# Performance work log

Hardware: AMD Instinct MI355X
Metric: run time of the kernel (lower is better)

Reference implementation:

```python
import jax, jax.numpy as jnp
import numpy as np

B, LQ, LK = 4, 2048, 2048
XS, YS, PD = 1024, 1024, 128


def setup_inputs() -> dict:
    key = jax.random.key(0)
    ks = jax.random.split(key, 8)
    s_x = 1.0 / np.sqrt(XS)
    s_y = 1.0 / np.sqrt(YS)
    return {
        "x": jax.random.normal(ks[0], (B, LQ, XS), dtype=jnp.float32),
        "y": jax.random.normal(ks[1], (B, LK, YS), dtype=jnp.float32),
        "Wq": jax.random.normal(ks[2], (XS, PD), dtype=jnp.float32) * s_x,
        "bq": jax.random.normal(ks[3], (PD,), dtype=jnp.float32) * 0.01,
        "Wk": jax.random.normal(ks[4], (YS, PD), dtype=jnp.float32) * s_y,
        "bk": jax.random.normal(ks[5], (PD,), dtype=jnp.float32) * 0.01,
        "Wv": jax.random.normal(ks[6], (YS, PD), dtype=jnp.float32) * s_y,
        "bv": jax.random.normal(ks[7], (PD,), dtype=jnp.float32) * 0.01,
        "mask": 1,
    }


def reference(x, y, Wq, bq, Wk, bk, Wv, bv, mask):
    # Projections (torch Linear: x @ W^T + b; here weights stored as [in, out])
    q = x @ Wq + bq  # [B, LQ, PD]
    k = y @ Wk + bk  # [B, LK, PD]
    v = y @ Wv + bv  # [B, LK, PD]
    scale = 1.0 / jnp.sqrt(jnp.asarray(PD, dtype=q.dtype))
    att = jax.nn.softmax(jnp.einsum("bqd,bkd->bqk", q, k) * scale, axis=-1)
    if mask:
        # NOTE: faithful to original — triu applied AFTER softmax (diagonal=1),
        # zeroing the lower triangle + diagonal without renormalizing.
        att = jnp.triu(att, k=1)
    return jnp.einsum("bqk,bkd->bqd", att, v)  # [B, LQ, PD]
```

## Files before the change

kernel.cpp:

```cpp
#include <hip/hip_runtime.h>

typedef short s8v __attribute__((ext_vector_type(8)));
typedef float f4v __attribute__((ext_vector_type(4)));

#define NB 4
#define LQ 2048
#define LKK 2048
#define XS 1024
#define PDD 128

#define PST 68
#define AST 132

__device__ __forceinline__ ushort f2bf(float x) {
  union { float f; uint u; } v; v.f = x;
  uint r = (v.u + 0x7fffu + ((v.u >> 16) & 1u)) >> 16;
  return (ushort)r;
}


__global__ __launch_bounds__(256) void k_wtrans(const float* __restrict__ Wq,
                                                const float* __restrict__ Wk,
                                                const float* __restrict__ Wv,
                                                ushort* __restrict__ Wt) {
  int p = blockIdx.y;
  const float* W = (p == 0) ? Wq : (p == 1) ? Wk : Wv;
  ushort* out = Wt + (size_t)p * (PDD * XS);
  int t = threadIdx.x;
  int n = t >> 1;
  int kk0 = (t & 1) * 16;
  int k0 = blockIdx.x * 32;
  ushort tmp[16];
#pragma unroll
  for (int i = 0; i < 16; ++i) tmp[i] = f2bf(W[(size_t)(k0 + kk0 + i) * PDD + n]);
  uint4 u0, u1;
  u0.x = tmp[0] | ((uint)tmp[1] << 16);  u0.y = tmp[2] | ((uint)tmp[3] << 16);
  u0.z = tmp[4] | ((uint)tmp[5] << 16);  u0.w = tmp[6] | ((uint)tmp[7] << 16);
  u1.x = tmp[8] | ((uint)tmp[9] << 16);  u1.y = tmp[10] | ((uint)tmp[11] << 16);
  u1.z = tmp[12] | ((uint)tmp[13] << 16); u1.w = tmp[14] | ((uint)tmp[15] << 16);
  int ct = n >> 4, lc = n & 15, kq = k0 >> 5;
  ushort* base = out + ((size_t)(ct * 32 + kq)) * 512 + (kk0 >> 3) * 128 + lc * 8;
  *(uint4*)base = u0;
  *(uint4*)(base + 128) = u1;
}

__global__ __launch_bounds__(256, 2) void k_proj(const float* __restrict__ x,
                                                 const float* __restrict__ y,
                                                 const ushort* __restrict__ Wt,
                                                 const float* __restrict__ bq,
                                                 const float* __restrict__ bk,
                                                 const float* __restrict__ bv,
                                                 ushort* __restrict__ qo,
                                                 ushort* __restrict__ ko,
                                                 ushort* __restrict__ vt) {
  __shared__ ushort As[32 * 1032];
  int bx = blockIdx.x;
  int xcd = bx & 7;
  int b = xcd >> 1;
  int half = xcd & 1;
  int idx = bx >> 3;
  int kind = idx & 1;
  int rt = (idx >> 1) + half * 32;
  int row0 = b * 2048 + rt * 32;
  const float* in = kind ? y : x;
  int t = threadIdx.x, wave = t >> 6, lane = t & 63, quad = lane >> 4, lc = lane & 15;

  {
    int c0 = t * 4;
    const float* src = in + (size_t)row0 * XS + c0;
#pragma unroll
    for (int rb = 0; rb < 4; ++rb) {
      float4 v0 = *(const float4*)(src + (size_t)(rb * 8 + 0) * XS);
      float4 v1 = *(const float4*)(src + (size_t)(rb * 8 + 1) * XS);
      float4 v2 = *(const float4*)(src + (size_t)(rb * 8 + 2) * XS);
      float4 v3 = *(const float4*)(src + (size_t)(rb * 8 + 3) * XS);
      float4 v4 = *(const float4*)(src + (size_t)(rb * 8 + 4) * XS);
      float4 v5 = *(const float4*)(src + (size_t)(rb * 8 + 5) * XS);
      float4 v6 = *(const float4*)(src + (size_t)(rb * 8 + 6) * XS);
      float4 v7 = *(const float4*)(src + (size_t)(rb * 8 + 7) * XS);
      uint2 pk;
#define STW(rr, vv)                                                        \
      pk.x = f2bf(vv.x) | ((uint)f2bf(vv.y) << 16);                        \
      pk.y = f2bf(vv.z) | ((uint)f2bf(vv.w) << 16);                        \
      *(uint2*)&As[(rb * 8 + rr) * 1032 + c0] = pk;
      STW(0, v0) STW(1, v1) STW(2, v2) STW(3, v3)
      STW(4, v4) STW(5, v5) STW(6, v6) STW(7, v7)
#undef STW
    }
  }
  __syncthreads();

  const f4v z4 = {0.f, 0.f, 0.f, 0.f};
  f4v acc0[2][2], acc1[2][2];
#pragma unroll
  for (int m = 0; m < 2; ++m)
#pragma unroll
    for (int n = 0; n < 2; ++n) { acc0[m][n] = z4; acc1[m][n] = z4; }

  const ushort* w0 = Wt + (size_t)(kind ? 1 : 0) * (PDD * XS) + lane * 8;
  const ushort* w1 = Wt + (size_t)2 * (PDD * XS) + lane * 8;
  int ct0 = wave * 2;

#pragma unroll 4
  for (int kq = 0; kq < 32; ++kq) {
    s8v a0 = *(const s8v*)&As[lc * 1032 + kq * 32 + quad * 8];
    s8v a1 = *(const s8v*)&As[(16 + lc) * 1032 + kq * 32 + quad * 8];
    s8v b00 = *(const s8v*)(w0 + ((size_t)(ct0 * 32 + kq)) * 512);
    s8v b01 = *(const s8v*)(w0 + ((size_t)((ct0 + 1) * 32 + kq)) * 512);
    acc0[0][0] = __builtin_amdgcn_mfma_f32_16x16x32_bf16(a0, b00, acc0[0][0], 0, 0, 0);
    acc0[0][1] = __builtin_amdgcn_mfma_f32_16x16x32_bf16(a0, b01, acc0[0][1], 0, 0, 0);
    acc0[1][0] = __builtin_amdgcn_mfma_f32_16x16x32_bf16(a1, b00, acc0[1][0], 0, 0, 0);
    acc0[1][1] = __builtin_amdgcn_mfma_f32_16x16x32_bf16(a1, b01, acc0[1][1], 0, 0, 0);
    if (kind) {
      s8v b10 = *(const s8v*)(w1 + ((size_t)(ct0 * 32 + kq)) * 512);
      s8v b11 = *(const s8v*)(w1 + ((size_t)((ct0 + 1) * 32 + kq)) * 512);
      acc1[0][0] = __builtin_amdgcn_mfma_f32_16x16x32_bf16(a0, b10, acc1[0][0], 0, 0, 0);
      acc1[0][1] = __builtin_amdgcn_mfma_f32_16x16x32_bf16(a0, b11, acc1[0][1], 0, 0, 0);
      acc1[1][0] = __builtin_amdgcn_mfma_f32_16x16x32_bf16(a1, b10, acc1[1][0], 0, 0, 0);
      acc1[1][1] = __builtin_amdgcn_mfma_f32_16x16x32_bf16(a1, b11, acc1[1][1], 0, 0, 0);
    }
  }

  const float qscale = 0.08838834764831845f;
  int rloc = rt * 32;
  if (kind == 0) {
#pragma unroll
    for (int m = 0; m < 2; ++m) {
      int qt = (rloc >> 4) + m;
#pragma unroll
      for (int n = 0; n < 2; ++n) {
        int col = wave * 32 + n * 16 + lc;
        float bb = bq[col];
        size_t base = ((((size_t)(b * 128 + qt) * 4 + wave) * 4 + (n * 2 + (lc >> 3))) * 16 +
                       quad * 4) * 8 + (lc & 7);
#pragma unroll
        for (int g = 0; g < 4; ++g)
          qo[base + (size_t)g * 8] = f2bf((acc0[m][n][g] + bb) * qscale);
      }
    }
  } else {
#pragma unroll
    for (int m = 0; m < 2; ++m) {
      int qt = (rloc >> 4) + m;
#pragma unroll
      for (int n = 0; n < 2; ++n) {
        int col = wave * 32 + n * 16 + lc;
        float bb = bk[col];
        size_t base = ((((size_t)(b * 128 + qt) * 4 + wave) * 4 + (n * 2 + (lc >> 3))) * 16 +
                       quad * 4) * 8 + (lc & 7);
#pragma unroll
        for (int g = 0; g < 4; ++g)
          ko[base + (size_t)g * 8] = f2bf(acc0[m][n][g] + bb);
      }
    }
#pragma unroll
    for (int m = 0; m < 2; ++m) {
      int rr = rloc + m * 16 + quad * 4;
      int kchunk = rr >> 5, qv = (rr >> 3) & 3, jj0 = rr & 7;
#pragma unroll
      for (int n = 0; n < 2; ++n) {
        int col = wave * 32 + n * 16 + lc;
        int dt = wave * 2 + n;
        float bb = bv[col];
        ushort4 pk;
        pk.x = f2bf(acc1[m][n][0] + bb);
        pk.y = f2bf(acc1[m][n][1] + bb);
        pk.z = f2bf(acc1[m][n][2] + bb);
        pk.w = f2bf(acc1[m][n][3] + bb);
        size_t off = ((((size_t)(b * 64 + kchunk) * 8 + dt) * 4 + qv) * 16 + lc) * 8 + jj0;
        *(ushort4*)&vt[off] = pk;
      }
    }
  }
}

__global__ __launch_bounds__(512, 2) void k_attn(const ushort* __restrict__ qg,
                                                 const ushort* __restrict__ kg,
                                                 const ushort* __restrict__ vtg,
                                                 const int* __restrict__ maskp,
                                                 float* __restrict__ out) {
  __shared__ float smem[8 * 32 * PST];
  __shared__ float lS[8][2][16];
  int bx = blockIdx.x;
  int xcd = bx & 7;
  int b = xcd >> 1;
  int q0 = ((bx >> 3) * 2 + (xcd & 1)) * 32;
  int t = threadIdx.x;
  int wave = t >> 6, lane = t & 63, quad = lane >> 4, lc = lane & 15;
  int domask = *maskp;
  float* Psw = smem + wave * (32 * PST);

  const ushort* qB = qg + ((size_t)(b * 128 + (q0 >> 4))) * 2048 + lane * 8;
  s8v aq[2][4];
#pragma unroll
  for (int m = 0; m < 2; ++m)
#pragma unroll
    for (int kc = 0; kc < 4; ++kc)
      aq[m][kc] = *(const s8v*)(qB + m * 2048 + kc * 512);

  const f4v z4 = {0.f, 0.f, 0.f, 0.f};
  f4v acc[2][8];
#pragma unroll
  for (int m = 0; m < 2; ++m)
#pragma unroll
    for (int i = 0; i < 8; ++i) acc[m][i] = z4;
  float rs[2][4] = {{0.f, 0.f, 0.f, 0.f}, {0.f, 0.f, 0.f, 0.f}};

#pragma unroll 1
  for (int i = 0; i < 4; ++i) {
    int kt = wave + i * 8;

    const ushort* kB = kg + ((size_t)(b * 128 + i * 32 + wave * 4)) * 2048 + lane * 8;
    s8v kf[16];
#pragma unroll
    for (int f = 0; f < 16; ++f) kf[f] = *(const s8v*)(kB + f * 512);

    f4v sf[2][4];
#pragma unroll
    for (int nt = 0; nt < 4; ++nt) {
      f4v s0 = z4, s1 = z4;
#pragma unroll
      for (int kc = 0; kc < 4; ++kc) {
        s0 = __builtin_amdgcn_mfma_f32_16x16x32_bf16(aq[0][kc], kf[nt * 4 + kc], s0, 0, 0, 0);
        s1 = __builtin_amdgcn_mfma_f32_16x16x32_bf16(aq[1][kc], kf[nt * 4 + kc], s1, 0, 0, 0);
      }
      sf[0][nt] = s0;
      sf[1][nt] = s1;
    }

    const ushort* vB = vtg + ((size_t)(b * 64 + i * 16 + wave * 2)) * 4096 + lane * 8;
    s8v vf[16];
#pragma unroll
    for (int f = 0; f < 16; ++f) vf[f] = *(const s8v*)(vB + f * 512);
    __builtin_amdgcn_sched_barrier(0);

#pragma unroll
    for (int m = 0; m < 2; ++m)
#pragma unroll
      for (int g = 0; g < 4; ++g) {
        int rg = q0 + m * 16 + quad * 4 + g;
#pragma unroll
        for (int nt = 0; nt < 4; ++nt) {
          float pv = __expf(sf[m][nt][g]);
          rs[m][g] += pv;
          int jg = kt * 64 + nt * 16 + lc;
          if (domask && (jg <= rg)) pv = 0.f;
          Psw[(m * 16 + quad * 4 + g) * PST + nt * 16 + lc] = pv;
        }
      }

#pragma unroll
    for (int jc = 0; jc < 2; ++jc)
#pragma unroll
      for (int m = 0; m < 2; ++m) {
        const float* pp = &Psw[(m * 16 + lc) * PST + jc * 32 + quad * 8];
        float4 p0 = *(const float4*)pp;
        float4 p1 = *(const float4*)(pp + 4);
        s8v ap;
        ap[0] = (short)f2bf(p0.x); ap[1] = (short)f2bf(p0.y);
        ap[2] = (short)f2bf(p0.z); ap[3] = (short)f2bf(p0.w);
        ap[4] = (short)f2bf(p1.x); ap[5] = (short)f2bf(p1.y);
        ap[6] = (short)f2bf(p1.z); ap[7] = (short)f2bf(p1.w);
#pragma unroll
        for (int dt = 0; dt < 8; ++dt) {
          acc[m][dt] = __builtin_amdgcn_mfma_f32_16x16x32_bf16(ap, vf[jc * 8 + dt], acc[m][dt], 0, 0, 0);
        }
      }
  }

#pragma unroll
  for (int off = 8; off >= 1; off >>= 1)
#pragma unroll
    for (int m = 0; m < 2; ++m)
#pragma unroll
      for (int g = 0; g < 4; ++g) rs[m][g] += __shfl_xor(rs[m][g], off, 64);

  __syncthreads();
  if (lc == 0) {
#pragma unroll
    for (int m = 0; m < 2; ++m)
#pragma unroll
      for (int g = 0; g < 4; ++g) lS[wave][m][quad * 4 + g] = rs[m][g];
  }

#pragma unroll
  for (int m = 0; m < 2; ++m) {
#pragma unroll
    for (int dt = 0; dt < 8; ++dt)
#pragma unroll
      for (int g = 0; g < 4; ++g)
        smem[wave * (16 * AST) + (quad * 4 + g) * AST + dt * 16 + lc] = acc[m][dt][g];
    __syncthreads();
    {
      int row = t >> 5, c0 = (t & 31) * 4;
      float L = 0.f;
      float ox = 0.f, oy = 0.f, oz = 0.f, ow = 0.f;
#pragma unroll
      for (int p = 0; p < 8; ++p) {
        L += lS[p][m][row];
        const float* a = &smem[p * (16 * AST) + row * AST + c0];
        float4 xv = *(const float4*)a;
        ox += xv.x; oy += xv.y; oz += xv.z; ow += xv.w;
      }
      float inv = 1.0f / L;
      float4 o;
      o.x = ox * inv; o.y = oy * inv; o.z = oz * inv; o.w = ow * inv;
      float* op = out + ((size_t)(b * LQ + q0 + m * 16 + row)) * PDD + c0;
      *(float4*)op = o;
    }
    __syncthreads();
  }
}

extern "C" void kernel_launch(void* const* d_in, const int* in_sizes, int n_in,
                              void* d_out, int out_size, void* d_ws, size_t ws_size,
                              hipStream_t stream) {
  const float* x  = (const float*)d_in[0];
  const float* y  = (const float*)d_in[1];
  const float* Wq = (const float*)d_in[2];
  const float* bq = (const float*)d_in[3];
  const float* Wk = (const float*)d_in[4];
  const float* bk = (const float*)d_in[5];
  const float* Wv = (const float*)d_in[6];
  const float* bv = (const float*)d_in[7];
  const int* mask = (const int*)d_in[8];
  char* ws = (char*)d_ws;
  ushort* qb = (ushort*)(ws);
  ushort* kb = (ushort*)(ws + (size_t)(1 << 21));
  ushort* vt = (ushort*)(ws + (size_t)(2 << 21));
  ushort* Wt = (ushort*)(ws + (size_t)(3 << 21));
  float* out = (float*)d_out;

  hipLaunchKernelGGL(k_wtrans, dim3(32, 3), dim3(256), 0, stream, Wq, Wk, Wv, Wt);
  hipLaunchKernelGGL(k_proj, dim3(512), dim3(256), 0, stream, x, y, Wt, bq, bk, bv, qb, kb, vt);
  hipLaunchKernelGGL(k_attn, dim3(256), dim3(512), 0, stream, qb, kb, vt, mask, out);
}
```

Before: 142.2 us.

## Load projection input tiles directly into LDS as fp32 and halve row tile

The projection kernel now stages 16-row fp32 input tiles straight into shared memory with global_load_lds, using an XOR swizzle against bank conflicts, instead of loading through registers and converting to bf16 before the store. Conversion to bf16 moves into the MFMA inner loop. The row tile shrinks from 32 to 16 and the grid doubles to 1024 blocks, so there are more, smaller blocks to improve occupancy and overlap. In exchange, every A fragment now costs extra conversion ALU work per k-step, and the shared Wt fragments are reloaded by twice as many blocks.

```diff
diff --git a/kernel.cpp b/kernel.cpp
--- a/kernel.cpp
+++ b/kernel.cpp
@@ -53,109 +53,88 @@
                                                  ushort* __restrict__ qo,
                                                  ushort* __restrict__ ko,
                                                  ushort* __restrict__ vt) {
-  __shared__ ushort As[32 * 1032];
+  __shared__ float As[16 * 1024];
   int bx = blockIdx.x;
   int xcd = bx & 7;
   int b = xcd >> 1;
   int half = xcd & 1;
   int idx = bx >> 3;
   int kind = idx & 1;
-  int rt = (idx >> 1) + half * 32;
-  int row0 = b * 2048 + rt * 32;
+  int rt = (idx >> 1) + half * 64;
+  int row0 = b * 2048 + rt * 16;
   const float* in = kind ? y : x;
   int t = threadIdx.x, wave = t >> 6, lane = t & 63, quad = lane >> 4, lc = lane & 15;
 
   {
-    int c0 = t * 4;
-    const float* src = in + (size_t)row0 * XS + c0;
-#pragma unroll
-    for (int rb = 0; rb < 4; ++rb) {
-      float4 v0 = *(const float4*)(src + (size_t)(rb * 8 + 0) * XS);
-      float4 v1 = *(const float4*)(src + (size_t)(rb * 8 + 1) * XS);
-      float4 v2 = *(const float4*)(src + (size_t)(rb * 8 + 2) * XS);
-      float4 v3 = *(const float4*)(src + (size_t)(rb * 8 + 3) * XS);
-      float4 v4 = *(const float4*)(src + (size_t)(rb * 8 + 4) * XS);
-      float4 v5 = *(const float4*)(src + (size_t)(rb * 8 + 5) * XS);
-      float4 v6 = *(const float4*)(src + (size_t)(rb * 8 + 6) * XS);
-      float4 v7 = *(const float4*)(src + (size_t)(rb * 8 + 7) * XS);
-      uint2 pk;
-#define STW(rr, vv)                                                        \
-      pk.x = f2bf(vv.x) | ((uint)f2bf(vv.y) << 16);                        \
-      pk.y = f2bf(vv.z) | ((uint)f2bf(vv.w) << 16);                        \
-      *(uint2*)&As[(rb * 8 + rr) * 1032 + c0] = pk;
-      STW(0, v0) STW(1, v1) STW(2, v2) STW(3, v3)
-      STW(4, v4) STW(5, v5) STW(6, v6) STW(7, v7)
-#undef STW
+    const char* tile = (const char*)(in + (size_t)row0 * XS);
+    char* lbase = (char*)As + wave * 1024;
+#pragma unroll
+    for (int i = 0; i < 16; ++i) {
+      const char* src = tile + i * 4096 + wave * 1024 + ((lane * 16) ^ ((i & 7) << 4));
+      __builtin_amdgcn_global_load_lds(
+          (const __attribute__((address_space(1))) uint*)src,
+          (__attribute__((address_space(3))) uint*)(lbase + i * 4096), 16, 0, 0);
     }
   }
   __syncthreads();
 
   const f4v z4 = {0.f, 0.f, 0.f, 0.f};
-  f4v acc0[2][2], acc1[2][2];
-#pragma unroll
-  for (int m = 0; m < 2; ++m)
-#pragma unroll
-    for (int n = 0; n < 2; ++n) { acc0[m][n] = z4; acc1[m][n] = z4; }
+  f4v acc0[2], acc1[2];
+  acc0[0] = z4; acc0[1] = z4; acc1[0] = z4; acc1[1] = z4;
 
   const ushort* w0 = Wt + (size_t)(kind ? 1 : 0) * (PDD * XS) + lane * 8;
   const ushort* w1 = Wt + (size_t)2 * (PDD * XS) + lane * 8;
   int ct0 = wave * 2;
+  int xorv = (lc & 7) << 2;
+  int fb0 = lc * 1024 + quad * 8;
 
 #pragma unroll 4
   for (int kq = 0; kq < 32; ++kq) {
-    s8v a0 = *(const s8v*)&As[lc * 1032 + kq * 32 + quad * 8];
-    s8v a1 = *(const s8v*)&As[(16 + lc) * 1032 + kq * 32 + quad * 8];
+    int fb = fb0 + kq * 32;
+    float4 lo = *(const float4*)&As[(fb) ^ xorv];
+    float4 hi = *(const float4*)&As[(fb + 4) ^ xorv];
+    s8v a;
+    a[0] = (short)f2bf(lo.x); a[1] = (short)f2bf(lo.y);
+    a[2] = (short)f2bf(lo.z); a[3] = (short)f2bf(lo.w);
+    a[4] = (short)f2bf(hi.x); a[5] = (short)f2bf(hi.y);
+    a[6] = (short)f2bf(hi.z); a[7] = (short)f2bf(hi.w);
     s8v b00 = *(const s8v*)(w0 + ((size_t)(ct0 * 32 + kq)) * 512);
     s8v b01 = *(const s8v*)(w0 + ((size_t)((ct0 + 1) * 32 + kq)) * 512);
-    acc0[0][0] = __builtin_amdgcn_mfma_f32_16x16x32_bf16(a0, b00, acc0[0][0], 0, 0, 0);
-    acc0[0][1] = __builtin_amdgcn_mfma_f32_16x16x32_bf16(a0, b01, acc0[0][1], 0, 0, 0);
-    acc0[1][0] = __builtin_amdgcn_mfma_f32_16x16x32_bf16(a1, b00, acc0[1][0], 0, 0, 0);
-    acc0[1][1] = __builtin_amdgcn_mfma_f32_16x16x32_bf16(a1, b01, acc0[1][1], 0, 0, 0);
+    acc0[0] = __builtin_amdgcn_mfma_f32_16x16x32_bf16(a, b00, acc0[0], 0, 0, 0);
+    acc0[1] = __builtin_amdgcn_mfma_f32_16x16x32_bf16(a, b01, acc0[1], 0, 0, 0);
     if (kind) {
       s8v b10 = *(const s8v*)(w1 + ((size_t)(ct0 * 32 + kq)) * 512);
       s8v b11 = *(const s8v*)(w1 + ((size_t)((ct0 + 1) * 32 + kq)) * 512);
-      acc1[0][0] = __builtin_amdgcn_mfma_f32_16x16x32_bf16(a0, b10, acc1[0][0], 0, 0, 0);
-      acc1[0][1] = __builtin_amdgcn_mfma_f32_16x16x32_bf16(a0, b11, acc1[0][1], 0, 0, 0);
-      acc1[1][0] = __builtin_amdgcn_mfma_f32_16x16x32_bf16(a1, b10, acc1[1][0], 0, 0, 0);
-      acc1[1][1] = __builtin_amdgcn_mfma_f32_16x16x32_bf16(a1, b11, acc1[1][1], 0, 0, 0);
+      acc1[0] = __builtin_amdgcn_mfma_f32_16x16x32_bf16(a, b10, acc1[0], 0, 0, 0);
+      acc1[1] = __builtin_amdgcn_mfma_f32_16x16x32_bf16(a, b11, acc1[1], 0, 0, 0);
     }
   }
 
   const float qscale = 0.08838834764831845f;
-  int rloc = rt * 32;
   if (kind == 0) {
 #pragma unroll
-    for (int m = 0; m < 2; ++m) {
-      int qt = (rloc >> 4) + m;
-#pragma unroll
-      for (int n = 0; n < 2; ++n) {
-        int col = wave * 32 + n * 16 + lc;
-        float bb = bq[col];
-        size_t base = ((((size_t)(b * 128 + qt) * 4 + wave) * 4 + (n * 2 + (lc >> 3))) * 16 +
-                       quad * 4) * 8 + (lc & 7);
-#pragma unroll
-        for (int g = 0; g < 4; ++g)
-          qo[base + (size_t)g * 8] = f2bf((acc0[m][n][g] + bb) * qscale);
-      }
+    for (int n = 0; n < 2; ++n) {
+      int col = wave * 32 + n * 16 + lc;
+      float bb = bq[col];
+      size_t base = ((((size_t)(b * 128 + rt) * 4 + wave) * 4 + (n * 2 + (lc >> 3))) * 16 +
+                     quad * 4) * 8 + (lc & 7);
+#pragma unroll
+      for (int g = 0; g < 4; ++g)
+        qo[base + (size_t)g * 8] = f2bf((acc0[n][g] + bb) * qscale);
     }
   } else {
 #pragma unroll
-    for (int m = 0; m < 2; ++m) {
-      int qt = (rloc >> 4) + m;
-#pragma unroll
-      for (int n = 0; n < 2; ++n) {
-        int col = wave * 32 + n * 16 + lc;
-        float bb = bk[col];
-        size_t base = ((((size_t)(b * 128 + qt) * 4 + wave) * 4 + (n * 2 + (lc >> 3))) * 16 +
-                       quad * 4) * 8 + (lc & 7);
-#pragma unroll
-        for (int g = 0; g < 4; ++g)
-          ko[base + (size_t)g * 8] = f2bf(acc0[m][n][g] + bb);
-      }
-    }
-#pragma unroll
-    for (int m = 0; m < 2; ++m) {
-      int rr = rloc + m * 16 + quad * 4;
+    for (int n = 0; n < 2; ++n) {
+      int col = wave * 32 + n * 16 + lc;
+      float bb = bk[col];
+      size_t base = ((((size_t)(b * 128 + rt) * 4 + wave) * 4 + (n * 2 + (lc >> 3))) * 16 +
+                     quad * 4) * 8 + (lc & 7);
+#pragma unroll
+      for (int g = 0; g < 4; ++g)
+        ko[base + (size_t)g * 8] = f2bf(acc0[n][g] + bb);
+    }
+    {
+      int rr = rt * 16 + quad * 4;
       int kchunk = rr >> 5, qv = (rr >> 3) & 3, jj0 = rr & 7;
 #pragma unroll
       for (int n = 0; n < 2; ++n) {
@@ -163,10 +142,10 @@
         int dt = wave * 2 + n;
         float bb = bv[col];
         ushort4 pk;
-        pk.x = f2bf(acc1[m][n][0] + bb);
-        pk.y = f2bf(acc1[m][n][1] + bb);
-        pk.z = f2bf(acc1[m][n][2] + bb);
-        pk.w = f2bf(acc1[m][n][3] + bb);
+        pk.x = f2bf(acc1[n][0] + bb);
+        pk.y = f2bf(acc1[n][1] + bb);
+        pk.z = f2bf(acc1[n][2] + bb);
+        pk.w = f2bf(acc1[n][3] + bb);
         size_t off = ((((size_t)(b * 64 + kchunk) * 8 + dt) * 4 + qv) * 16 + lc) * 8 + jj0;
         *(ushort4*)&vt[off] = pk;
       }
@@ -332,6 +311,6 @@
   float* out = (float*)d_out;
 
   hipLaunchKernelGGL(k_wtrans, dim3(32, 3), dim3(256), 0, stream, Wq, Wk, Wv, Wt);
-  hipLaunchKernelGGL(k_proj, dim3(512), dim3(256), 0, stream, x, y, Wt, bq, bk, bv, qb, kb, vt);
+  hipLaunchKernelGGL(k_proj, dim3(1024), dim3(256), 0, stream, x, y, Wt, bq, bk, bv, qb, kb, vt);
   hipLaunchKernelGGL(k_attn, dim3(256), dim3(512), 0, stream, qb, kb, vt, mask, out);
 }
```

New measurement: 174.0 us. 1.22x slower.
